# Optimization experiments

Hardware: AMD Instinct MI355X
Metric: run time of the kernel (lower is better)

Reference implementation:

```python
import jax, jax.numpy as jnp
import numpy as np
from jax import lax

EPS = 1e-5

def _conv3x3(x, w):
    # x: [N,C,H,W], w: [O,I,3,3]
    return lax.conv_general_dilated(x, w, window_strides=(1, 1),
                                    padding=((1, 1), (1, 1)),
                                    dimension_numbers=('NCHW', 'OIHW', 'NCHW'))

def _bn(x, gamma, beta, mean, var):
    # inference-mode batchnorm, per-channel over dim 1
    scale = (gamma * lax.rsqrt(var + EPS))[None, :, None, None]
    shift = (beta - mean * gamma * lax.rsqrt(var + EPS))[None, :, None, None]
    return x * scale + shift

def setup_inputs() -> dict:
    key = jax.random.key(0)
    ks = jax.random.split(key, 11)
    N, C, H, W = 64, 128, 56, 56
    d = {}
    d['x'] = jax.random.normal(ks[0], (N, C, H, W), dtype=jnp.float32)
    d['w1'] = jax.random.normal(ks[1], (C, C, 3, 3), dtype=jnp.float32) * (1.0 / np.sqrt(9 * C))
    d['g1'] = jax.random.uniform(ks[2], (C,), dtype=jnp.float32, minval=0.5, maxval=1.5)
    d['b1'] = jax.random.normal(ks[3], (C,), dtype=jnp.float32) * 0.1
    d['m1'] = jax.random.normal(ks[4], (C,), dtype=jnp.float32) * 0.1
    d['v1'] = jax.random.uniform(ks[5], (C,), dtype=jnp.float32, minval=0.5, maxval=1.5)
    d['w2'] = jax.random.normal(ks[6], (C, C, 3, 3), dtype=jnp.float32) * (1.0 / np.sqrt(9 * C))
    d['g2'] = jax.random.uniform(ks[7], (C,), dtype=jnp.float32, minval=0.5, maxval=1.5)
    d['b2'] = jax.random.normal(ks[8], (C,), dtype=jnp.float32) * 0.1
    d['m2'] = jax.random.normal(ks[9], (C,), dtype=jnp.float32) * 0.1
    d['v2'] = jax.random.uniform(ks[10], (C,), dtype=jnp.float32, minval=0.5, maxval=1.5)
    return d

def reference(x, w1, g1, b1, m1, v1, w2, g2, b2, m2, v2):
    identity = x  # downsample is None (stride=1, inplanes==planes)
    out = _conv3x3(x, w1)
    out = jax.nn.relu(_bn(out, g1, b1, m1, v1))
    out = _conv3x3(out, w2)
    out = _bn(out, g2, b2, m2, v2)
    out = out + identity
    return jax.nn.relu(out)
```

## Files before the change

kernel.cpp:

```cpp
#include <hip/hip_runtime.h>
#include <hip/hip_bf16.h>

typedef __attribute__((ext_vector_type(8))) short short8;
typedef __attribute__((ext_vector_type(4))) float f32x4;

static constexpr int NN = 64;
static constexpr int C  = 128;
static constexpr int H  = 56;
static constexpr int W  = 56;
static constexpr int HP = 58;
static constexpr int KTOT = 1152;

__device__ __forceinline__ void gload16(const void* g, void* l) {
    __builtin_amdgcn_global_load_lds(
        (const __attribute__((address_space(1))) unsigned int*)g,
        (__attribute__((address_space(3))) unsigned int*)l, 16, 0, 0);
}

__global__ __launch_bounds__(128)
void pack_weights(const float* __restrict__ w, const float* __restrict__ g,
                  const float* __restrict__ b, const float* __restrict__ m,
                  const float* __restrict__ v, __hip_bfloat16* __restrict__ Wp,
                  float* __restrict__ shift)
{
    int o = blockIdx.x;
    int c = threadIdx.x;
    float scale = g[o] * rsqrtf(v[o] + 1e-5f);
    if (c == 0) shift[o] = b[o] - m[o] * scale;
    const float* ws = w + ((size_t)o * C + c) * 9;
    #pragma unroll
    for (int tap = 0; tap < 9; ++tap)
        Wp[(size_t)o * KTOT + tap * C + c] = __float2bfloat16(ws[tap] * scale);
}

__global__ __launch_bounds__(256)
void transform_x(const float* __restrict__ x, __hip_bfloat16* __restrict__ Xp)
{
    __shared__ float t[C * 57];
    int bid = blockIdx.x;
    int n = bid / H, h = bid % H;
    int tid = threadIdx.x;

    #pragma unroll
    for (int i = 0; i < 7; ++i) {
        int idx4 = i * 256 + tid;
        int c  = idx4 / 14;
        int wq = (idx4 % 14) * 4;
        const float* p = x + ((size_t)(n * C + c)) * (H * W) + h * W + wq;
        float4 vv = *(const float4*)p;
        t[c * 57 + wq + 0] = vv.x;
        t[c * 57 + wq + 1] = vv.y;
        t[c * 57 + wq + 2] = vv.z;
        t[c * 57 + wq + 3] = vv.w;
    }
    __syncthreads();
    #pragma unroll
    for (int i = 0; i < 28; ++i) {
        int idx = i * 256 + tid;
        int c = idx & 127, w = idx >> 7;
        float vv = t[c * 57 + w];
        Xp[(((size_t)n * HP + (h + 1)) * HP + (w + 1)) * C + c] = __float2bfloat16(vv);
    }
}

template<int WHICH>
__global__ __launch_bounds__(256)
void conv3x3_kernel(const __hip_bfloat16* __restrict__ Xp,
                    const __hip_bfloat16* __restrict__ Wp,
                    const float* __restrict__ shift,
                    const float* __restrict__ ident,
                    void* __restrict__ outp)
{
    __shared__ char s_x[68 * 256];
    __shared__ char s_w[128 * 256];

    const int tid  = threadIdx.x;
    const int wave = tid >> 6;
    const int lane = tid & 63;
    const int lr = lane & 15, lg = lane >> 4;

    const int bid = blockIdx.x;
    const int n = bid / H, h = bid % H;

    const char* xrow0 = (const char*)Xp + ((size_t)n * HP + h) * (HP * 256);

    f32x4 acc[8];
    #pragma unroll
    for (int i = 0; i < 8; ++i) acc[i] = (f32x4){0.f, 0.f, 0.f, 0.f};

    for (int kh = 0; kh < 3; ++kh) {
        const char* xs = xrow0 + kh * (HP * 256);
        for (int blk = wave; blk < 17; blk += 4) {
            int dst = blk * 1024 + lane * 16;
            int src = dst ^ (((dst >> 8) & 7) << 4);
            gload16(xs + src, s_x + blk * 1024);
        }
        for (int kw = 0; kw < 3; ++kw) {
            const int tap = kh * 3 + kw;
            const char* wt = (const char*)Wp + tap * 256;
            #pragma unroll
            for (int i = 0; i < 8; ++i) {
                int blk = wave * 8 + i;
                int dst = blk * 1024 + lane * 16;
                int o   = dst >> 8;
                int col = (dst & 255) ^ ((o & 7) << 4);
                gload16(wt + (size_t)o * (KTOT * 2) + col, s_w + blk * 1024);
            }
            __syncthreads();

            #pragma unroll
            for (int kb = 0; kb < 4; ++kb) {
                const int cb = kb * 64 + lg * 16;
                short8 xa[4], wb[2];
                #pragma unroll
                for (int sm = 0; sm < 4; ++sm) {
                    int row = sm * 16 + lr + kw;
                    int off = ((row << 8) + cb) ^ ((row & 7) << 4);
                    xa[sm] = *(const short8*)(s_x + off);
                }
                #pragma unroll
                for (int so = 0; so < 2; ++so) {
                    int o = wave * 32 + so * 16 + lr;
                    int off = ((o << 8) + cb) ^ ((o & 7) << 4);
                    wb[so] = *(const short8*)(s_w + off);
                }
                #pragma unroll
                for (int sm = 0; sm < 4; ++sm)
                    #pragma unroll
                    for (int so = 0; so < 2; ++so) {
                        if (WHICH == 0)
                            acc[sm * 2 + so] = __builtin_amdgcn_mfma_f32_16x16x32_bf16(
                                xa[sm], wb[so], acc[sm * 2 + so], 0, 0, 0);
                        else
                            acc[so * 4 + sm] = __builtin_amdgcn_mfma_f32_16x16x32_bf16(
                                wb[so], xa[sm], acc[so * 4 + sm], 0, 0, 0);
                    }
            }
            __syncthreads();
        }
    }

    if (WHICH == 0) {
        __hip_bfloat16* o1 = (__hip_bfloat16*)outp;
        size_t rowbase = ((size_t)n * HP + (h + 1)) * HP;
        #pragma unroll
        for (int so = 0; so < 2; ++so) {
            int o = wave * 32 + so * 16 + lr;
            float sh = shift[o];
            #pragma unroll
            for (int sm = 0; sm < 4; ++sm) {
                f32x4 vv = acc[sm * 2 + so];
                #pragma unroll
                for (int r = 0; r < 4; ++r) {
                    int m = sm * 16 + lg * 4 + r;
                    if (m < W) {
                        float f = vv[r] + sh;
                        f = f > 0.f ? f : 0.f;
                        o1[(rowbase + (m + 1)) * C + o] = __float2bfloat16(f);
                    }
                }
            }
        }
    } else {
        float* o2 = (float*)outp;
        #pragma unroll
        for (int so = 0; so < 2; ++so) {
            int obase = wave * 32 + so * 16 + lg * 4;
            f32x4 sh4 = *(const f32x4*)(shift + obase);
            #pragma unroll
            for (int sm = 0; sm < 4; ++sm) {
                f32x4 vv = acc[so * 4 + sm];
                int m = sm * 16 + lr;
                if (m < W) {
                    #pragma unroll
                    for (int r = 0; r < 4; ++r) {
                        int o = obase + r;
                        size_t idx = ((size_t)(n * C + o) * H + h) * W + m;
                        float f = vv[r] + sh4[r] + ident[idx];
                        o2[idx] = f > 0.f ? f : 0.f;
                    }
                }
            }
        }
    }
}

extern "C" void kernel_launch(void* const* d_in, const int* in_sizes, int n_in,
                              void* d_out, int out_size, void* d_ws, size_t ws_size,
                              hipStream_t stream)
{
    const float* x  = (const float*)d_in[0];
    const float* w1 = (const float*)d_in[1];
    const float* g1 = (const float*)d_in[2];
    const float* b1 = (const float*)d_in[3];
    const float* m1 = (const float*)d_in[4];
    const float* v1 = (const float*)d_in[5];
    const float* w2 = (const float*)d_in[6];
    const float* g2 = (const float*)d_in[7];
    const float* b2 = (const float*)d_in[8];
    const float* m2 = (const float*)d_in[9];
    const float* v2 = (const float*)d_in[10];
    float* out = (float*)d_out;

    char* ws = (char*)d_ws;
    const size_t PADBUF = (size_t)NN * HP * HP * C * 2;
    size_t oX  = 0;
    size_t oY  = oX + PADBUF + 32768;
    size_t oW1 = oY + PADBUF + 32768;
    size_t oW2 = oW1 + (size_t)C * KTOT * 2;
    size_t oS1 = oW2 + (size_t)C * KTOT * 2;
    size_t oS2 = oS1 + 512;

    __hip_bfloat16* Xp  = (__hip_bfloat16*)(ws + oX);
    __hip_bfloat16* Y1  = (__hip_bfloat16*)(ws + oY);
    __hip_bfloat16* W1p = (__hip_bfloat16*)(ws + oW1);
    __hip_bfloat16* W2p = (__hip_bfloat16*)(ws + oW2);
    float* s1 = (float*)(ws + oS1);
    float* s2 = (float*)(ws + oS2);

    hipMemsetAsync(Xp, 0, PADBUF, stream);
    hipMemsetAsync(Y1, 0, PADBUF, stream);

    pack_weights<<<128, 128, 0, stream>>>(w1, g1, b1, m1, v1, W1p, s1);
    pack_weights<<<128, 128, 0, stream>>>(w2, g2, b2, m2, v2, W2p, s2);
    transform_x<<<NN * H, 256, 0, stream>>>(x, Xp);

    conv3x3_kernel<0><<<NN * H, 256, 0, stream>>>(Xp, W1p, s1, nullptr, (void*)Y1);
    conv3x3_kernel<1><<<NN * H, 256, 0, stream>>>(Y1, W2p, s2, x, (void*)out);
}
```

Measured before the change: 236.1 us.

## Compute two output rows per block with rolling input-row LDS buffers

Each workgroup now produces two adjacent output rows. Every weight tile loaded into LDS feeds twice as many MFMAs, which halves weight traffic per output, and the grid shrinks to match. Input rows sit in a two-slot rotating LDS buffer, so each padded input row is loaded once and reused across the kh taps, and the XOR swizzle widens from 8 to 16 rows. The cost is doubled accumulator registers. Reads for the masked tail columns can now go past the 64-row input slot into neighbouring LDS; this only touches outputs that are thrown away.

```diff
diff --git a/kernel.cpp b/kernel.cpp
--- a/kernel.cpp
+++ b/kernel.cpp
@@ -71,7 +71,7 @@
                     const float* __restrict__ ident,
                     void* __restrict__ outp)
 {
-    __shared__ char s_x[68 * 256];
+    __shared__ char s_x[2][64 * 256];
     __shared__ char s_w[128 * 256];
 
     const int tid  = threadIdx.x;
@@ -80,21 +80,24 @@
     const int lr = lane & 15, lg = lane >> 4;
 
     const int bid = blockIdx.x;
-    const int n = bid / H, h = bid % H;
-
-    const char* xrow0 = (const char*)Xp + ((size_t)n * HP + h) * (HP * 256);
-
-    f32x4 acc[8];
-    #pragma unroll
-    for (int i = 0; i < 8; ++i) acc[i] = (f32x4){0.f, 0.f, 0.f, 0.f};
+    const int n = bid / 28, h0 = (bid % 28) * 2;
+
+    const char* xbase = (const char*)Xp + ((size_t)n * HP + h0) * (HP * 256);
+
+    #pragma unroll
+    for (int i = 0; i < 8; ++i) {
+        int t = wave + i * 4;
+        int q = t >> 4, blk = t & 15;
+        int dst = blk * 1024 + lane * 16;
+        int src = dst ^ (((dst >> 8) & 15) << 4);
+        gload16(xbase + (size_t)q * (HP * 256) + src, s_x[q] + blk * 1024);
+    }
+
+    f32x4 acc[16];
+    #pragma unroll
+    for (int i = 0; i < 16; ++i) acc[i] = (f32x4){0.f, 0.f, 0.f, 0.f};
 
     for (int kh = 0; kh < 3; ++kh) {
-        const char* xs = xrow0 + kh * (HP * 256);
-        for (int blk = wave; blk < 17; blk += 4) {
-            int dst = blk * 1024 + lane * 16;
-            int src = dst ^ (((dst >> 8) & 7) << 4);
-            gload16(xs + src, s_x + blk * 1024);
-        }
         for (int kw = 0; kw < 3; ++kw) {
             const int tap = kh * 3 + kw;
             const char* wt = (const char*)Wp + tap * 256;
@@ -103,7 +106,7 @@
                 int blk = wave * 8 + i;
                 int dst = blk * 1024 + lane * 16;
                 int o   = dst >> 8;
-                int col = (dst & 255) ^ ((o & 7) << 4);
+                int col = (dst & 255) ^ ((o & 15) << 4);
                 gload16(wt + (size_t)o * (KTOT * 2) + col, s_w + blk * 1024);
             }
             __syncthreads();
@@ -111,52 +114,64 @@
             #pragma unroll
             for (int kb = 0; kb < 4; ++kb) {
                 const int cb = kb * 64 + lg * 16;
-                short8 xa[4], wb[2];
-                #pragma unroll
-                for (int sm = 0; sm < 4; ++sm) {
-                    int row = sm * 16 + lr + kw;
-                    int off = ((row << 8) + cb) ^ ((row & 7) << 4);
-                    xa[sm] = *(const short8*)(s_x + off);
+                short8 xa[8], wb[2];
+                #pragma unroll
+                for (int sm = 0; sm < 8; ++sm) {
+                    int row  = (sm & 3) * 16 + lr + kw;
+                    int slot = (kh + (sm >> 2)) & 1;
+                    int off  = ((row << 8) + cb) ^ ((row & 15) << 4);
+                    xa[sm] = *(const short8*)(s_x[slot] + off);
                 }
                 #pragma unroll
                 for (int so = 0; so < 2; ++so) {
-                    int o = wave * 32 + so * 16 + lr;
-                    int off = ((o << 8) + cb) ^ ((o & 7) << 4);
+                    int o   = wave * 32 + so * 16 + lr;
+                    int off = ((o << 8) + cb) ^ ((o & 15) << 4);
                     wb[so] = *(const short8*)(s_w + off);
                 }
                 #pragma unroll
-                for (int sm = 0; sm < 4; ++sm)
+                for (int sm = 0; sm < 8; ++sm)
                     #pragma unroll
                     for (int so = 0; so < 2; ++so) {
                         if (WHICH == 0)
                             acc[sm * 2 + so] = __builtin_amdgcn_mfma_f32_16x16x32_bf16(
                                 xa[sm], wb[so], acc[sm * 2 + so], 0, 0, 0);
                         else
-                            acc[so * 4 + sm] = __builtin_amdgcn_mfma_f32_16x16x32_bf16(
-                                wb[so], xa[sm], acc[so * 4 + sm], 0, 0, 0);
+                            acc[so * 8 + sm] = __builtin_amdgcn_mfma_f32_16x16x32_bf16(
+                                wb[so], xa[sm], acc[so * 8 + sm], 0, 0, 0);
                     }
             }
             __syncthreads();
+        }
+        if (kh < 2) {
+            #pragma unroll
+            for (int i = 0; i < 4; ++i) {
+                int blk = wave + i * 4;
+                int dst = blk * 1024 + lane * 16;
+                int src = dst ^ (((dst >> 8) & 15) << 4);
+                gload16(xbase + (size_t)(kh + 2) * (HP * 256) + src,
+                        s_x[kh & 1] + blk * 1024);
+            }
         }
     }
 
     if (WHICH == 0) {
         __hip_bfloat16* o1 = (__hip_bfloat16*)outp;
-        size_t rowbase = ((size_t)n * HP + (h + 1)) * HP;
         #pragma unroll
         for (int so = 0; so < 2; ++so) {
             int o = wave * 32 + so * 16 + lr;
             float sh = shift[o];
             #pragma unroll
-            for (int sm = 0; sm < 4; ++sm) {
+            for (int sm = 0; sm < 8; ++sm) {
                 f32x4 vv = acc[sm * 2 + so];
+                int out_r = sm >> 2;
+                size_t rowbase = ((size_t)n * HP + (h0 + out_r + 1)) * HP;
                 #pragma unroll
                 for (int r = 0; r < 4; ++r) {
-                    int m = sm * 16 + lg * 4 + r;
-                    if (m < W) {
+                    int w = (sm & 3) * 16 + lg * 4 + r;
+                    if (w < W) {
                         float f = vv[r] + sh;
                         f = f > 0.f ? f : 0.f;
-                        o1[(rowbase + (m + 1)) * C + o] = __float2bfloat16(f);
+                        o1[(rowbase + (w + 1)) * C + o] = __float2bfloat16(f);
                     }
                 }
             }
@@ -168,14 +183,15 @@
             int obase = wave * 32 + so * 16 + lg * 4;
             f32x4 sh4 = *(const f32x4*)(shift + obase);
             #pragma unroll
-            for (int sm = 0; sm < 4; ++sm) {
-                f32x4 vv = acc[so * 4 + sm];
-                int m = sm * 16 + lr;
-                if (m < W) {
+            for (int sm = 0; sm < 8; ++sm) {
+                f32x4 vv = acc[so * 8 + sm];
+                int w = (sm & 3) * 16 + lr;
+                int h = h0 + (sm >> 2);
+                if (w < W) {
                     #pragma unroll
                     for (int r = 0; r < 4; ++r) {
                         int o = obase + r;
-                        size_t idx = ((size_t)(n * C + o) * H + h) * W + m;
+                        size_t idx = ((size_t)(n * C + o) * H + h) * W + w;
                         float f = vv[r] + sh4[r] + ident[idx];
                         o2[idx] = f > 0.f ? f : 0.f;
                     }
@@ -225,6 +241,6 @@
     pack_weights<<<128, 128, 0, stream>>>(w2, g2, b2, m2, v2, W2p, s2);
     transform_x<<<NN * H, 256, 0, stream>>>(x, Xp);
 
-    conv3x3_kernel<0><<<NN * H, 256, 0, stream>>>(Xp, W1p, s1, nullptr, (void*)Y1);
-    conv3x3_kernel<1><<<NN * H, 256, 0, stream>>>(Y1, W2p, s2, x, (void*)out);
-}
+    conv3x3_kernel<0><<<NN * 28, 256, 0, stream>>>(Xp, W1p, s1, nullptr, (void*)Y1);
+    conv3x3_kernel<1><<<NN * 28, 256, 0, stream>>>(Y1, W2p, s2, x, (void*)out);
+}
```

After: 302.2 us. 28.0% more time.
